# Kernel tuning notes

Measured on AMD Instinct MI355X. Metric: run time of the kernel, lower is better.

## Reference

```python
import jax, jax.numpy as jnp
import numpy as np

ALPHA = 0.2  # LeakyReLU negative slope


def setup_inputs() -> dict:
    key = jax.random.key(0)
    k1, k2, k3, k4 = jax.random.split(key, 4)
    N, E, d_in, d_out = 100000, 1600000, 64, 64
    node_features = jax.random.normal(k1, (N, d_in), dtype=jnp.float32)
    edge_index = jax.random.randint(k2, (2, E), 0, N, dtype=jnp.int64)
    # learned params: W is Linear(in,out,bias=False) weight used as x @ W.T; store as [d_in,d_out]
    W = jax.random.normal(k3, (d_in, d_out), dtype=jnp.float32) * (1.414 * np.sqrt(2.0 / (d_in + d_out)))
    a = jax.random.normal(k4, (2 * d_out,), dtype=jnp.float32) * (1.414 * np.sqrt(2.0 / (2 * d_out + 1)))
    return {"node_features": node_features, "edge_index": edge_index, "W": W, "a": a}


def reference(node_features, edge_index, W, a):
    N = node_features.shape[0]
    d_out = W.shape[1]
    src, tgt = edge_index[0], edge_index[1]

    h = node_features @ W  # [N, d_out]
    # a([h_src, h_tgt]) == h_src @ a[:d] + h_tgt @ a[d:]; compute node-level scores once
    s_src = h @ a[:d_out]   # [N]
    s_tgt = h @ a[d_out:]   # [N]
    e = jax.nn.leaky_relu(s_src[src] + s_tgt[tgt], negative_slope=ALPHA)  # [E]

    # per-target segment softmax (stable): scatter-max, exp, scatter-sum
    m = jax.ops.segment_max(e, tgt, num_segments=N)          # [N]
    e_exp = jnp.exp(e - m[tgt])                              # [E]
    denom = jax.ops.segment_sum(e_exp, tgt, num_segments=N)  # [N]
    attention = e_exp / denom[tgt]                           # [E]
    # dropout is identity in eval mode (training=False)

    # weighted scatter-add of source features into targets
    h_prime = jax.ops.segment_sum(h[src] * attention[:, None], tgt, num_segments=N)  # [N, d_out]
    return jax.nn.elu(h_prime)
```

## Files before the change

### kernel.cpp

```cpp
#include <hip/hip_runtime.h>
#include <hip/hip_bf16.h>
#include <math.h>

#define ALPHA  0.2f
#define BSH    6
#define BNODES 64
#define NBMAX  1600
#define K_CH   4096
#define CAPB   2048
#define SCH    7

static __device__ __forceinline__ unsigned short f2bf(float x) {
    __hip_bfloat16 b = __float2bfloat16(x);
    return *reinterpret_cast<unsigned short*>(&b);
}

__global__ __launch_bounds__(256) void k_prep(
    const float* __restrict__ X, const float* __restrict__ W,
    const float* __restrict__ a, unsigned short* __restrict__ hb,
    float* __restrict__ s_src, float* __restrict__ s_tgt,
    const int* __restrict__ src, const int* __restrict__ tgt,
    int* __restrict__ cur, int* __restrict__ ebuf,
    int N, int E, int nb, int gFill)
{
    __shared__ __align__(16) char smem[37632];
    const int tid = threadIdx.x;

    if (blockIdx.x >= gFill) {
        float (*Xs)[65] = (float(*)[65])smem;
        float (*Ws)[64] = (float(*)[64])(smem + 16640);
        const int row0 = (blockIdx.x - gFill) * 64;

        {
            const float4* W4 = (const float4*)W;
            float4* Wd = (float4*)&Ws[0][0];
            for (int q = tid; q < 1024; q += 256) Wd[q] = W4[q];
        }
        for (int q = tid; q < 1024; q += 256) {
            int r  = q >> 4;
            int c4 = (q & 15) * 4;
            int row = row0 + r;
            float4 v = make_float4(0.f, 0.f, 0.f, 0.f);
            if (row < N) v = *(const float4*)&X[(size_t)row * 64 + c4];
            Xs[r][c4 + 0] = v.x; Xs[r][c4 + 1] = v.y;
            Xs[r][c4 + 2] = v.z; Xs[r][c4 + 3] = v.w;
        }
        __syncthreads();

        const int cg = (tid & 7) * 8;
        const int rg = (tid >> 3) * 2;

        float acc[2][8];
#pragma unroll
        for (int r = 0; r < 2; ++r)
#pragma unroll
            for (int c = 0; c < 8; ++c) acc[r][c] = 0.f;

#pragma unroll 8
        for (int k = 0; k < 64; ++k) {
            float4 wv0 = *(const float4*)&Ws[k][cg];
            float4 wv1 = *(const float4*)&Ws[k][cg + 4];
            float x0 = Xs[rg + 0][k];
            float x1 = Xs[rg + 1][k];
            acc[0][0] += x0 * wv0.x; acc[0][1] += x0 * wv0.y;
            acc[0][2] += x0 * wv0.z; acc[0][3] += x0 * wv0.w;
            acc[0][4] += x0 * wv1.x; acc[0][5] += x0 * wv1.y;
            acc[0][6] += x0 * wv1.z; acc[0][7] += x0 * wv1.w;
            acc[1][0] += x1 * wv0.x; acc[1][1] += x1 * wv0.y;
            acc[1][2] += x1 * wv0.z; acc[1][3] += x1 * wv0.w;
            acc[1][4] += x1 * wv1.x; acc[1][5] += x1 * wv1.y;
            acc[1][6] += x1 * wv1.z; acc[1][7] += x1 * wv1.w;
        }

        float a1v[8], a2v[8];
#pragma unroll
        for (int c = 0; c < 8; ++c) { a1v[c] = a[cg + c]; a2v[c] = a[64 + cg + c]; }

#pragma unroll
        for (int r = 0; r < 2; ++r) {
            int row = row0 + rg + r;
            if (row < N) {
                uint4 hv;
                hv.x = (unsigned)f2bf(acc[r][0]) | ((unsigned)f2bf(acc[r][1]) << 16);
                hv.y = (unsigned)f2bf(acc[r][2]) | ((unsigned)f2bf(acc[r][3]) << 16);
                hv.z = (unsigned)f2bf(acc[r][4]) | ((unsigned)f2bf(acc[r][5]) << 16);
                hv.w = (unsigned)f2bf(acc[r][6]) | ((unsigned)f2bf(acc[r][7]) << 16);
                *(uint4*)&hb[(size_t)row * 64 + cg] = hv;
            }
            float v1 = 0.f, v2 = 0.f;
#pragma unroll
            for (int c = 0; c < 8; ++c) {
                v1 += acc[r][c] * a1v[c];
                v2 += acc[r][c] * a2v[c];
            }
            v1 += __shfl_xor(v1, 1); v2 += __shfl_xor(v2, 1);
            v1 += __shfl_xor(v1, 2); v2 += __shfl_xor(v2, 2);
            v1 += __shfl_xor(v1, 4); v2 += __shfl_xor(v2, 4);
            if ((tid & 7) == 0 && row < N) { s_src[row] = v1; s_tgt[row] = v2; }
        }
    } else {
        int* pk    = (int*)smem;
        int* hist  = (int*)(smem + 16384);
        int* off_s = (int*)(smem + 22784);
        int* gbase = (int*)(smem + 29184);
        int* part  = (int*)(smem + 35584);

        const int blk = blockIdx.x;
        const int e0  = blk * K_CH;
        const int e1  = min(e0 + K_CH, E);
        const int cnt = e1 - e0;

        for (int i = tid; i < nb; i += 256) hist[i] = 0;
        __syncthreads();

        {
            const int4* t4 = (const int4*)tgt;
            const int v0 = e0 >> 2, v1e = e1 >> 2;
            for (int i = v0 + tid; i < v1e; i += 256) {
                int4 v = t4[i];
                atomicAdd(&hist[v.x >> BSH], 1);
                atomicAdd(&hist[v.y >> BSH], 1);
                atomicAdd(&hist[v.z >> BSH], 1);
                atomicAdd(&hist[v.w >> BSH], 1);
            }
            for (int i = (e1 & ~3) + tid; i < e1; i += 256)
                atomicAdd(&hist[tgt[i] >> BSH], 1);
        }
        __syncthreads();

        int pref[SCH];
        {
            int s = 0;
            const int i0 = tid * SCH;
#pragma unroll
            for (int j = 0; j < SCH; ++j) {
                int idx = i0 + j;
                int v = (idx < nb) ? hist[idx] : 0;
                pref[j] = s;
                s += v;
            }
            part[tid] = s;
        }
        __syncthreads();
#pragma unroll
        for (int o = 1; o < 256; o <<= 1) {
            int t2 = (tid >= o) ? part[tid - o] : 0;
            __syncthreads();
            part[tid] += t2;
            __syncthreads();
        }
        {
            const int base0 = (tid > 0) ? part[tid - 1] : 0;
            const int i0 = tid * SCH;
#pragma unroll
            for (int j = 0; j < SCH; ++j) {
                int idx = i0 + j;
                if (idx < nb) off_s[idx] = base0 + pref[j];
            }
        }
        __syncthreads();

        for (int i = tid; i < nb; i += 256) {
            int c = hist[i];
            if (c) {
                int within = atomicAdd(&cur[i], c);
                gbase[i] = i * CAPB + within;
            }
            hist[i] = off_s[i];
        }
        __syncthreads();

        {
            const int4* t4 = (const int4*)tgt;
            const int4* s4 = (const int4*)src;
            const int v0 = e0 >> 2, v1e = e1 >> 2;
            for (int i = v0 + tid; i < v1e; i += 256) {
                int4 tv = t4[i];
                int4 sv = s4[i];
                int b0 = tv.x >> BSH, p0 = atomicAdd(&hist[b0], 1);
                pk[p0] = sv.x | ((tv.x & (BNODES - 1)) << 17);
                int b1 = tv.y >> BSH, p1 = atomicAdd(&hist[b1], 1);
                pk[p1] = sv.y | ((tv.y & (BNODES - 1)) << 17);
                int b2 = tv.z >> BSH, p2 = atomicAdd(&hist[b2], 1);
                pk[p2] = sv.z | ((tv.z & (BNODES - 1)) << 17);
                int b3 = tv.w >> BSH, p3 = atomicAdd(&hist[b3], 1);
                pk[p3] = sv.w | ((tv.w & (BNODES - 1)) << 17);
            }
            for (int i = (e1 & ~3) + tid; i < e1; i += 256) {
                int t = tgt[i];
                int b = t >> BSH;
                int p = atomicAdd(&hist[b], 1);
                pk[p] = src[i] | ((t & (BNODES - 1)) << 17);
            }
        }
        __syncthreads();

        for (int i = tid; i < cnt; i += 256) {
            int lo = 0, hi = nb;
            while (hi - lo > 1) {
                int mid = (lo + hi) >> 1;
                if (off_s[mid] <= i) lo = mid; else hi = mid;
            }
            int rel = i - off_s[lo];
            int gb  = gbase[lo];
            if ((gb & (CAPB - 1)) + rel < CAPB) ebuf[gb + rel] = pk[i];
        }
    }
}

__global__ __launch_bounds__(256) void k_bgather(
    const int* __restrict__ cur, const int* __restrict__ ebuf,
    const float* __restrict__ s_src, const float* __restrict__ s_tgt,
    const uint2* __restrict__ hb2,
    float* __restrict__ out, int N)
{
    __shared__ uint2 spe[CAPB];
    __shared__ int   hist[BNODES];
    __shared__ int   off_s[BNODES + 1];
    __shared__ int   cur_s[BNODES];
    __shared__ float sT[BNODES];

    const int tid  = threadIdx.x;
    const int b    = blockIdx.x;
    const int base = b << BSH;
    const int nn   = min(BNODES, N - base);
    const int beg  = b * CAPB;
    const int cnt  = min(cur[b], CAPB);

    if (tid < BNODES) {
        hist[tid] = 0;
        sT[tid] = (base + tid < N) ? s_tgt[base + tid] : 0.f;
    }
    __syncthreads();

    int pkr[8];
#pragma unroll
    for (int j = 0; j < 8; ++j) {
        int i = tid + j * 256;
        pkr[j] = (i < cnt) ? ebuf[beg + i] : -1;
        if (pkr[j] >= 0) atomicAdd(&hist[(pkr[j] >> 17) & (BNODES - 1)], 1);
    }
    __syncthreads();

    if (tid < 64) {
        int v = hist[tid];
        int incl = v;
#pragma unroll
        for (int o = 1; o < 64; o <<= 1) {
            int t2 = __shfl_up(incl, o);
            if (tid >= o) incl += t2;
        }
        off_s[tid + 1] = incl;
        cur_s[tid]     = incl - v;
        if (tid == 0) off_s[0] = 0;
    }
    __syncthreads();

#pragma unroll
    for (int j = 0; j < 8; ++j) {
        int pkv = pkr[j];
        if (pkv >= 0) {
            int toff = (pkv >> 17) & (BNODES - 1);
            int sv   = pkv & 0x1FFFF;
            int pos  = atomicAdd(&cur_s[toff], 1);
            float sc = s_src[sv] + sT[toff];
            sc = (sc >= 0.f) ? sc : ALPHA * sc;
            spe[pos] = make_uint2((unsigned)sv << 4,
                                  __float_as_uint(__expf(sc)));
        }
    }
    __syncthreads();

    const int w     = tid >> 6;
    const int lane  = tid & 63;
    const int g     = lane >> 4;
    const int fidx2 = lane & 15;

    for (int tl = w; tl < nn; tl += 4) {
        const int t    = base + tl;
        const int beg2 = off_s[tl];
        const int c    = off_s[tl + 1] - beg2;
        const unsigned ocol = (unsigned)t * 64 + fidx2 * 4;

        if (c == 0) {
            if (g == 0) *(float4*)&out[ocol] = make_float4(0.f, 0.f, 0.f, 0.f);
            continue;
        }

        float ax = 0.f, ay = 0.f, az = 0.f, aw = 0.f, den = 0.f;
        for (int k = 0; k < c; k += 8) {
            int idx0 = k + g;
            int idx1 = k + 4 + g;
            int cl0  = beg2 + min(idx0, c - 1);
            int cl1  = beg2 + min(idx1, c - 1);
            uint2 m0 = spe[cl0];
            uint2 m1 = spe[cl1];
            uint2 u0 = hb2[m0.x + fidx2];
            uint2 u1 = hb2[m1.x + fidx2];
            float p0 = (idx0 < c) ? __uint_as_float(m0.y) : 0.f;
            float p1 = (idx1 < c) ? __uint_as_float(m1.y) : 0.f;
            den += p0;
            ax += p0 * __uint_as_float(u0.x << 16);
            ay += p0 * __uint_as_float(u0.x & 0xFFFF0000u);
            az += p0 * __uint_as_float(u0.y << 16);
            aw += p0 * __uint_as_float(u0.y & 0xFFFF0000u);
            den += p1;
            ax += p1 * __uint_as_float(u1.x << 16);
            ay += p1 * __uint_as_float(u1.x & 0xFFFF0000u);
            az += p1 * __uint_as_float(u1.y << 16);
            aw += p1 * __uint_as_float(u1.y & 0xFFFF0000u);
        }
        ax += __shfl_xor(ax, 16); ay += __shfl_xor(ay, 16);
        az += __shfl_xor(az, 16); aw += __shfl_xor(aw, 16);
        den += __shfl_xor(den, 16);
        ax += __shfl_xor(ax, 32); ay += __shfl_xor(ay, 32);
        az += __shfl_xor(az, 32); aw += __shfl_xor(aw, 32);
        den += __shfl_xor(den, 32);

        if (g == 0) {
            float rd = 1.f / den;
            float r0 = ax * rd, r1 = ay * rd, r2 = az * rd, r3 = aw * rd;
            r0 = (r0 > 0.f) ? r0 : expm1f(r0);
            r1 = (r1 > 0.f) ? r1 : expm1f(r1);
            r2 = (r2 > 0.f) ? r2 : expm1f(r2);
            r3 = (r3 > 0.f) ? r3 : expm1f(r3);
            *(float4*)&out[ocol] = make_float4(r0, r1, r2, r3);
        }
    }
}

extern "C" void kernel_launch(void* const* d_in, const int* in_sizes, int n_in,
                              void* d_out, int out_size, void* d_ws, size_t ws_size,
                              hipStream_t stream)
{
    const float* X  = (const float*)d_in[0];
    const int*   ei = (const int*)d_in[1];
    const float* W  = (const float*)d_in[2];
    const float* a  = (const float*)d_in[3];

    const int N = in_sizes[0] / 64;
    const int E = in_sizes[1] / 2;
    const int* src = ei;
    const int* tgt = ei + E;

    float* out = (float*)d_out;

    const int nb    = (N + BNODES - 1) >> BSH;
    const int nbA   = (N + 63) / 64;
    const int gFill = (E + K_CH - 1) / K_CH;

    char* ws = (char*)d_ws;
    unsigned short* hb = (unsigned short*)ws; ws += (size_t)N * 64 * sizeof(unsigned short);
    float* s_src  = (float*)ws; ws += (size_t)N * sizeof(float);
    float* s_tgt  = (float*)ws; ws += (size_t)N * sizeof(float);
    int*   cur    = (int*)ws;   ws += (size_t)nb * sizeof(int);
    int*   ebuf   = (int*)ws;   ws += (size_t)nb * CAPB * sizeof(int);

    hipMemsetAsync(cur, 0, (size_t)nb * sizeof(int), stream);

    k_prep    <<<gFill + nbA, 256, 0, stream>>>(X, W, a, hb, s_src, s_tgt,
                                                src, tgt, cur, ebuf, N, E, nb, gFill);
    k_bgather <<<nb, 256, 0, stream>>>(cur, ebuf, s_src, s_tgt,
                                       (const uint2*)hb, out, N);
}
```

Baseline: 100.4 us.

## Compute node projection with bf16 MFMA instead of scalar FP32 FMAs

Replaces the scalar FP32 64x64 matmul in the prep kernel with bf16 MFMA 16x16x32 instructions. X and W are converted to bf16 into XOR-swizzled shared memory, attention scores are reduced from the accumulator fragments, and h is staged through shared memory for coalesced writes. This lowers ALU cost in the GEMM part but rounds the inputs to bf16, which reduces the precision of h and of the scores. The GEMM is likely a small share of a pipeline dominated by edge work.

```diff
diff --git a/kernel.cpp b/kernel.cpp
--- a/kernel.cpp
+++ b/kernel.cpp
@@ -9,6 +9,9 @@
 #define K_CH   4096
 #define CAPB   2048
 #define SCH    7
+
+typedef __attribute__((ext_vector_type(8))) short bf16x8;
+typedef __attribute__((ext_vector_type(4))) float f32x4;
 
 static __device__ __forceinline__ unsigned short f2bf(float x) {
     __hip_bfloat16 b = __float2bfloat16(x);
@@ -27,76 +30,104 @@
     const int tid = threadIdx.x;
 
     if (blockIdx.x >= gFill) {
-        float (*Xs)[65] = (float(*)[65])smem;
-        float (*Ws)[64] = (float(*)[64])(smem + 16640);
         const int row0 = (blockIdx.x - gFill) * 64;
 
-        {
-            const float4* W4 = (const float4*)W;
-            float4* Wd = (float4*)&Ws[0][0];
-            for (int q = tid; q < 1024; q += 256) Wd[q] = W4[q];
-        }
         for (int q = tid; q < 1024; q += 256) {
             int r  = q >> 4;
             int c4 = (q & 15) * 4;
             int row = row0 + r;
             float4 v = make_float4(0.f, 0.f, 0.f, 0.f);
             if (row < N) v = *(const float4*)&X[(size_t)row * 64 + c4];
-            Xs[r][c4 + 0] = v.x; Xs[r][c4 + 1] = v.y;
-            Xs[r][c4 + 2] = v.z; Xs[r][c4 + 3] = v.w;
-        }
-        __syncthreads();
-
-        const int cg = (tid & 7) * 8;
-        const int rg = (tid >> 3) * 2;
-
-        float acc[2][8];
-#pragma unroll
-        for (int r = 0; r < 2; ++r)
-#pragma unroll
-            for (int c = 0; c < 8; ++c) acc[r][c] = 0.f;
-
-#pragma unroll 8
-        for (int k = 0; k < 64; ++k) {
-            float4 wv0 = *(const float4*)&Ws[k][cg];
-            float4 wv1 = *(const float4*)&Ws[k][cg + 4];
-            float x0 = Xs[rg + 0][k];
-            float x1 = Xs[rg + 1][k];
-            acc[0][0] += x0 * wv0.x; acc[0][1] += x0 * wv0.y;
-            acc[0][2] += x0 * wv0.z; acc[0][3] += x0 * wv0.w;
-            acc[0][4] += x0 * wv1.x; acc[0][5] += x0 * wv1.y;
-            acc[0][6] += x0 * wv1.z; acc[0][7] += x0 * wv1.w;
-            acc[1][0] += x1 * wv0.x; acc[1][1] += x1 * wv0.y;
-            acc[1][2] += x1 * wv0.z; acc[1][3] += x1 * wv0.w;
-            acc[1][4] += x1 * wv1.x; acc[1][5] += x1 * wv1.y;
-            acc[1][6] += x1 * wv1.z; acc[1][7] += x1 * wv1.w;
-        }
-
-        float a1v[8], a2v[8];
-#pragma unroll
-        for (int c = 0; c < 8; ++c) { a1v[c] = a[cg + c]; a2v[c] = a[64 + cg + c]; }
-
-#pragma unroll
-        for (int r = 0; r < 2; ++r) {
-            int row = row0 + rg + r;
-            if (row < N) {
-                uint4 hv;
-                hv.x = (unsigned)f2bf(acc[r][0]) | ((unsigned)f2bf(acc[r][1]) << 16);
-                hv.y = (unsigned)f2bf(acc[r][2]) | ((unsigned)f2bf(acc[r][3]) << 16);
-                hv.z = (unsigned)f2bf(acc[r][4]) | ((unsigned)f2bf(acc[r][5]) << 16);
-                hv.w = (unsigned)f2bf(acc[r][6]) | ((unsigned)f2bf(acc[r][7]) << 16);
-                *(uint4*)&hb[(size_t)row * 64 + cg] = hv;
-            }
-            float v1 = 0.f, v2 = 0.f;
-#pragma unroll
-            for (int c = 0; c < 8; ++c) {
-                v1 += acc[r][c] * a1v[c];
-                v2 += acc[r][c] * a2v[c];
-            }
-            v1 += __shfl_xor(v1, 1); v2 += __shfl_xor(v2, 1);
-            v1 += __shfl_xor(v1, 2); v2 += __shfl_xor(v2, 2);
-            v1 += __shfl_xor(v1, 4); v2 += __shfl_xor(v2, 4);
-            if ((tid & 7) == 0 && row < N) { s_src[row] = v1; s_tgt[row] = v2; }
+            ushort4 bv;
+            bv.x = f2bf(v.x); bv.y = f2bf(v.y); bv.z = f2bf(v.z); bv.w = f2bf(v.w);
+            unsigned byte = (unsigned)r * 128 + (unsigned)c4 * 2;
+            byte ^= (unsigned)(r & 7) << 4;
+            *(ushort4*)(smem + byte) = bv;
+        }
+        for (int q = tid; q < 1024; q += 256) {
+            int k  = q >> 4;
+            int n0 = (q & 15) * 4;
+            float4 v = *(const float4*)&W[k * 64 + n0];
+            float vv[4] = {v.x, v.y, v.z, v.w};
+#pragma unroll
+            for (int i = 0; i < 4; ++i) {
+                int n = n0 + i;
+                unsigned byte = 8192u + (unsigned)n * 128 + (unsigned)k * 2;
+                byte ^= (unsigned)(n & 7) << 4;
+                *(unsigned short*)(smem + byte) = f2bf(vv[i]);
+            }
+        }
+        __syncthreads();
+
+        const int wv   = tid >> 6;
+        const int l    = tid & 63;
+        const int lrow = l & 15;
+        const int lk   = (l >> 4) * 8;
+
+        auto frag = [&](unsigned base, int row, int k) -> bf16x8 {
+            unsigned byte = base + (unsigned)row * 128 + (unsigned)k * 2;
+            byte ^= (unsigned)(row & 7) << 4;
+            return *(const bf16x8*)(smem + byte);
+        };
+
+        bf16x8 a0 = frag(0u, wv * 16 + lrow, lk);
+        bf16x8 a1 = frag(0u, wv * 16 + lrow, 32 + lk);
+
+        f32x4 acc[4];
+#pragma unroll
+        for (int t = 0; t < 4; ++t) acc[t] = (f32x4){0.f, 0.f, 0.f, 0.f};
+
+#pragma unroll
+        for (int t = 0; t < 4; ++t) {
+            bf16x8 b0 = frag(8192u, t * 16 + lrow, lk);
+            bf16x8 b1 = frag(8192u, t * 16 + lrow, 32 + lk);
+            acc[t] = __builtin_amdgcn_mfma_f32_16x16x32_bf16(a0, b0, acc[t], 0, 0, 0);
+            acc[t] = __builtin_amdgcn_mfma_f32_16x16x32_bf16(a1, b1, acc[t], 0, 0, 0);
+        }
+
+        float s1p[4] = {0.f, 0.f, 0.f, 0.f};
+        float s2p[4] = {0.f, 0.f, 0.f, 0.f};
+#pragma unroll
+        for (int t = 0; t < 4; ++t) {
+            float a1c = a[t * 16 + lrow];
+            float a2c = a[64 + t * 16 + lrow];
+#pragma unroll
+            for (int r = 0; r < 4; ++r) {
+                s1p[r] += acc[t][r] * a1c;
+                s2p[r] += acc[t][r] * a2c;
+            }
+        }
+#pragma unroll
+        for (int r = 0; r < 4; ++r) {
+            s1p[r] += __shfl_xor(s1p[r], 1); s2p[r] += __shfl_xor(s2p[r], 1);
+            s1p[r] += __shfl_xor(s1p[r], 2); s2p[r] += __shfl_xor(s2p[r], 2);
+            s1p[r] += __shfl_xor(s1p[r], 4); s2p[r] += __shfl_xor(s2p[r], 4);
+            s1p[r] += __shfl_xor(s1p[r], 8); s2p[r] += __shfl_xor(s2p[r], 8);
+        }
+        if (lrow == 0) {
+#pragma unroll
+            for (int r = 0; r < 4; ++r) {
+                int row = row0 + wv * 16 + (l >> 4) * 4 + r;
+                if (row < N) { s_src[row] = s1p[r]; s_tgt[row] = s2p[r]; }
+            }
+        }
+
+        __syncthreads();
+#pragma unroll
+        for (int t = 0; t < 4; ++t)
+#pragma unroll
+            for (int r = 0; r < 4; ++r) {
+                int row = wv * 16 + (l >> 4) * 4 + r;
+                int col = t * 16 + lrow;
+                *(unsigned short*)(smem + (unsigned)row * 128 + (unsigned)col * 2)
+                    = f2bf(acc[t][r]);
+            }
+        __syncthreads();
+        for (int q = tid; q < 512; q += 256) {
+            int row = q >> 3;
+            int gr  = row0 + row;
+            if (gr < N)
+                ((uint4*)&hb[(size_t)gr * 64])[q & 7] = ((const uint4*)smem)[q];
         }
     } else {
         int* pk    = (int*)smem;
```

Measured after the change: 103.1 us. 2.7% more time.
